# Kernel tuning notes

Hardware: AMD Instinct MI355X
Metric: run time of the kernel (lower is better)

The kernel has to match this reference:

```python
import jax, jax.numpy as jnp
import numpy as np

N = 50000      # nodes
E = 800000     # edges
IN = 64        # in_feats
HID = 4        # hidden_size
OUT = 64       # out_feats
COORS = 3
EPS = 1e-07
NEG_SLOPE = 0.01  # F.leaky_relu default


def setup_inputs() -> dict:
    key = jax.random.key(0)
    ks = jax.random.split(key, 10)
    feat = jax.random.normal(ks[0], (N, IN), dtype=jnp.float32)
    pos = jax.random.normal(ks[1], (N, COORS), dtype=jnp.float32)
    src = jax.random.randint(ks[2], (E,), 0, N, dtype=jnp.int32)
    dst = jax.random.randint(ks[3], (E,), 0, N, dtype=jnp.int32)
    W_self = jax.random.normal(ks[4], (OUT, IN), dtype=jnp.float32) * 0.1
    W_sp = jax.random.normal(ks[5], (HID * IN, COORS), dtype=jnp.float32) * 0.3
    b_sp = jax.random.normal(ks[6], (HID * IN,), dtype=jnp.float32) * 0.05
    W_neigh = jax.random.normal(ks[7], (OUT, HID * IN), dtype=jnp.float32) * 0.05
    b_neigh = jax.random.normal(ks[8], (OUT,), dtype=jnp.float32) * 0.05
    bias = jnp.zeros((OUT,), dtype=jnp.float32)
    return {"feat": feat, "pos": pos, "src": src, "dst": dst,
            "W_self": W_self, "W_sp": W_sp, "b_sp": b_sp,
            "W_neigh": W_neigh, "b_neigh": b_neigh, "bias": bias}


def reference(feat, pos, src, dst, W_self, W_sp, b_sp, W_neigh, b_neigh, bias):
    # per-edge spatial weighting
    rel = pos[dst] - pos[src]                                   # [E, 3]
    scal = jnp.linalg.norm(rel, axis=1, keepdims=True) + EPS    # [E, 1]
    ws = (rel + 1.0) / scal                                     # [E, 3]
    s = jax.nn.leaky_relu(ws @ W_sp.T + b_sp, NEG_SLOPE)        # [E, HID*IN]
    # modulate gathered src features: reshape(E, IN, HID) * h_src[:, :, None]
    msg = (s.reshape(E, IN, HID) * feat[src][:, :, None]).reshape(E, IN * HID)
    # mean aggregation per destination node (zero for isolated nodes)
    neigh_sum = jax.ops.segment_sum(msg, dst, num_segments=N)   # [N, IN*HID]
    cnt = jax.ops.segment_sum(jnp.ones((E,), feat.dtype), dst, num_segments=N)
    neigh_h = neigh_sum / jnp.maximum(cnt, 1.0)[:, None]
    # output projections
    h_neigh = neigh_h @ W_neigh.T + b_neigh                     # [N, OUT]
    rst = feat @ W_self.T + h_neigh + bias                      # [N, OUT]
    return rst
```

## Files before the change

kernel.cpp:

```cpp
#include <hip/hip_runtime.h>
#include <math.h>

#define N_NODES 50000
#define N_EDGES 800000
#define EPS 1e-7f
#define NEG_SLOPE 0.01f

#define BUCKET 64
#define GSTRIDE 72
#define EDGE_BLOCKS (N_EDGES / 256)
#define FEAT_BLOCKS (N_NODES * 64 / 4 / 256)

typedef __attribute__((ext_vector_type(8))) short short8;
typedef __attribute__((ext_vector_type(4))) float f32x4;

__device__ __forceinline__ unsigned bf16_rne(float x) {
    unsigned u = __float_as_uint(x);
    u += 0x7fffu + ((u >> 16) & 1u);
    return u >> 16;
}
__device__ __forceinline__ unsigned pack_bf16(float a, float b) {
    return bf16_rne(a) | (bf16_rne(b) << 16);
}


__global__ __launch_bounds__(256) void hist_geom_kernel(
    const int* __restrict__ src, const int* __restrict__ dst,
    const float* __restrict__ pos, int* __restrict__ cnt,
    uint2* __restrict__ gdata)
{
    const int i = blockIdx.x * 256 + threadIdx.x;
    const int s = src[i], d = dst[i];
    const float sx = pos[s * 3 + 0], sy = pos[s * 3 + 1], sz = pos[s * 3 + 2];
    const float dx = pos[d * 3 + 0], dy = pos[d * 3 + 1], dz = pos[d * 3 + 2];
    const float rx = dx - sx, ry = dy - sy, rz = dz - sz;
    const float inv =
        __builtin_amdgcn_rcpf(__builtin_amdgcn_sqrtf(rx * rx + ry * ry + rz * rz) + EPS);
    const uint2 rec = make_uint2(pack_bf16((rx + 1.f) * inv, (ry + 1.f) * inv),
                                 bf16_rne((rz + 1.f) * inv) | ((unsigned)s << 16));
    const int p = atomicAdd(&cnt[d], 1);
    if (p < BUCKET) gdata[(size_t)d * GSTRIDE + p] = rec;
}


__global__ __launch_bounds__(256) void featpack_kernel(
    const float* __restrict__ feat, uint2* __restrict__ featb2,
    const float* __restrict__ W_neigh, const float* __restrict__ W_self,
    const float* __restrict__ b_neigh, const float* __restrict__ bias,
    unsigned* __restrict__ wnp, unsigned* __restrict__ wsp, float* __restrict__ bb)
{
    const int bid = blockIdx.x;
    if (bid == FEAT_BLOCKS) {
        const int t = threadIdx.x;
        const float2* Wn2 = (const float2*)W_neigh;
        const float2* Ws2 = (const float2*)W_self;
        for (int i = t; i < 64 * 128; i += 256) {
            float2 v = Wn2[i];
            wnp[i] = pack_bf16(v.x, v.y);
        }
        for (int i = t; i < 64 * 32; i += 256) {
            float2 v = Ws2[i];
            wsp[i] = pack_bf16(v.x, v.y);
        }
        if (t < 64) bb[t] = b_neigh[t] + bias[t];
        return;
    }
    const int idx = bid * 256 + threadIdx.x;
    float4 v = reinterpret_cast<const float4*>(feat)[idx];
    featb2[idx] = make_uint2(pack_bf16(v.x, v.y), pack_bf16(v.z, v.w));
}


#define ACC_STRIDE 264

__device__ __forceinline__ float featload(const unsigned short* featb, unsigned rec_y, int lane) {
    return __uint_as_float((unsigned)featb[(size_t)(rec_y >> 16) * 64 + lane] << 16);
}

__global__ __launch_bounds__(256) void aggregate_project_kernel(
    const unsigned short* __restrict__ featb, const float* __restrict__ W_sp,
    const float* __restrict__ b_sp, const int* __restrict__ cnt,
    const uint2* __restrict__ gdata, const short* __restrict__ wnb,
    const short* __restrict__ wsb, const float* __restrict__ bb,
    float* __restrict__ out)
{
    __shared__ unsigned short accS[16 * ACC_STRIDE];
    __shared__ uint2 recS[16 * GSTRIDE];

    const int lane = threadIdx.x & 63;
    const int w = threadIdx.x >> 6;
    const int nb = blockIdx.x << 4;

    {
        const uint2* gsrc = gdata + (size_t)nb * GSTRIDE;
        for (int i = threadIdx.x; i < 16 * GSTRIDE; i += 256) recS[i] = gsrc[i];
    }

    float wsp0[4], wsp1[4], wsp2[4], bsp[4];
#pragma unroll
    for (int h = 0; h < 4; ++h) {
        int j = lane * 4 + h;
        wsp0[h] = W_sp[j * 3 + 0];
        wsp1[h] = W_sp[j * 3 + 1];
        wsp2[h] = W_sp[j * 3 + 2];
        bsp[h]  = b_sp[j];
    }
    __syncthreads();

#define MLP_ACC(U, F)                                                              \
    {                                                                              \
        const float wx = __uint_as_float((U).x << 16);                             \
        const float wy = __uint_as_float((U).x & 0xffff0000u);                     \
        const float wz = __uint_as_float((U).y << 16);                             \
        float t0 = fmaf(wx, wsp0[0], fmaf(wy, wsp1[0], fmaf(wz, wsp2[0], bsp[0])));\
        float t1 = fmaf(wx, wsp0[1], fmaf(wy, wsp1[1], fmaf(wz, wsp2[1], bsp[1])));\
        float t2 = fmaf(wx, wsp0[2], fmaf(wy, wsp1[2], fmaf(wz, wsp2[2], bsp[2])));\
        float t3 = fmaf(wx, wsp0[3], fmaf(wy, wsp1[3], fmaf(wz, wsp2[3], bsp[3])));\
        a0 = fmaf(fmaxf(t0, t0 * NEG_SLOPE), (F), a0);                             \
        a1 = fmaf(fmaxf(t1, t1 * NEG_SLOPE), (F), a1);                             \
        a2 = fmaf(fmaxf(t2, t2 * NEG_SLOPE), (F), a2);                             \
        a3 = fmaf(fmaxf(t3, t3 * NEG_SLOPE), (F), a3);                             \
    }

    for (int q = 0; q < 4; ++q) {
        const int r = (w << 2) + q;
        const int n = nb + r;
        const int degt = __builtin_amdgcn_readfirstlane(cnt[n]);
        const int deg = min(degt, BUCKET);
        const uint2* gp = &recS[r * GSTRIDE];

        float a0 = 0.f, a1 = 0.f, a2 = 0.f, a3 = 0.f;

        if (deg > 0) {
            const int dm = deg - 1;
            uint2 u0 = gp[0];
            uint2 u1 = gp[1];
            float f0 = featload(featb, u0.y, lane);
            float f1 = featload(featb, u1.y, lane);

            for (int e = 0; e < deg; e += 2) {
                uint2 u2 = gp[e + 2];
                uint2 u3 = gp[e + 3];
                float f2 = featload(featb, u2.y, lane);
                float f3 = featload(featb, u3.y, lane);

                MLP_ACC(u0, f0)
                {
                    const float fm = (e + 1 <= dm) ? f1 : 0.f;
                    MLP_ACC(u1, fm)
                }

                u0 = u2; u1 = u3;
                f0 = f2; f1 = f3;
            }
        }

        const float mscale = 1.f / fmaxf((float)degt, 1.f);
        uint2 pv = make_uint2(pack_bf16(a0 * mscale, a1 * mscale),
                              pack_bf16(a2 * mscale, a3 * mscale));
        *reinterpret_cast<uint2*>(&accS[r * ACC_STRIDE + lane * 4]) = pv;
    }
#undef MLP_ACC
    __syncthreads();

    const int mrow = lane & 15;
    const int quad = lane >> 4;
    const int o = (w << 4) + mrow;

    f32x4 acc = {0.f, 0.f, 0.f, 0.f};

    const unsigned short* Ar = &accS[mrow * ACC_STRIDE + quad * 8];
    const short* Br = wnb + o * 256 + quad * 8;
#pragma unroll
    for (int ks = 0; ks < 8; ++ks) {
        short8 a = *reinterpret_cast<const short8*>(Ar + ks * 32);
        short8 b = *reinterpret_cast<const short8*>(Br + ks * 32);
        acc = __builtin_amdgcn_mfma_f32_16x16x32_bf16(a, b, acc, 0, 0, 0);
    }

    const short* Fr = (const short*)featb + (size_t)(nb + mrow) * 64 + quad * 8;
    const short* Sr = wsb + o * 64 + quad * 8;
#pragma unroll
    for (int ks = 0; ks < 2; ++ks) {
        short8 a = *reinterpret_cast<const short8*>(Fr + ks * 32);
        short8 b = *reinterpret_cast<const short8*>(Sr + ks * 32);
        acc = __builtin_amdgcn_mfma_f32_16x16x32_bf16(a, b, acc, 0, 0, 0);
    }

    const float badd = bb[o];
#pragma unroll
    for (int r = 0; r < 4; ++r) {
        out[(size_t)(nb + quad * 4 + r) * 64 + o] = acc[r] + badd;
    }
}


extern "C" void kernel_launch(void* const* d_in, const int* in_sizes, int n_in,
                              void* d_out, int out_size, void* d_ws, size_t ws_size,
                              hipStream_t stream) {
    (void)in_sizes; (void)n_in; (void)out_size; (void)ws_size;
    const float* feat    = (const float*)d_in[0];
    const float* pos     = (const float*)d_in[1];
    const int*   src     = (const int*)d_in[2];
    const int*   dst     = (const int*)d_in[3];
    const float* W_self  = (const float*)d_in[4];
    const float* W_sp    = (const float*)d_in[5];
    const float* b_sp    = (const float*)d_in[6];
    const float* W_neigh = (const float*)d_in[7];
    const float* b_neigh = (const float*)d_in[8];
    const float* bias    = (const float*)d_in[9];
    float* out = (float*)d_out;

    uint2*        gdata  = (uint2*)d_ws;
    uint2*        featb2 = gdata + (size_t)N_NODES * GSTRIDE;
    unsigned int* wnp    = (unsigned int*)(featb2 + 800000);
    unsigned int* wsp    = wnp + 8192;
    float*        bb     = (float*)(wsp + 2048);
    int*          cnt    = (int*)(bb + 64);

    hipMemsetAsync(cnt, 0, (size_t)N_NODES * sizeof(int), stream);
    featpack_kernel<<<FEAT_BLOCKS + 1, 256, 0, stream>>>(
        feat, featb2, W_neigh, W_self, b_neigh, bias, wnp, wsp, bb);
    hist_geom_kernel<<<EDGE_BLOCKS, 256, 0, stream>>>(src, dst, pos, cnt, gdata);
    aggregate_project_kernel<<<N_NODES / 16, 256, 0, stream>>>(
        (const unsigned short*)featb2, W_sp, b_sp, cnt, gdata,
        (const short*)wnp, (const short*)wsp, bb, out);
}
```

Baseline: 185.1 us.

## Store 16-bit source ids in buckets and compute edge geometry in aggregation

The histogram pass now scatters only a 16-bit source index per edge instead of an 8-byte record with precomputed geometry. The relative-position weighting is recomputed inside the aggregation kernel, one edge per lane, and staged in shared memory. The feature-pack and histogram kernels are also merged into a single launch. This shrinks the random scatter traffic and the bucket reads and drops one launch, at the cost of extra pos gathers and math in the aggregation kernel.

```diff
diff --git a/kernel.cpp b/kernel.cpp
--- a/kernel.cpp
+++ b/kernel.cpp
@@ -8,8 +8,9 @@
 
 #define BUCKET 64
 #define GSTRIDE 72
+#define FEAT_BLOCKS (N_NODES * 64 / 4 / 256)
 #define EDGE_BLOCKS (N_EDGES / 256)
-#define FEAT_BLOCKS (N_NODES * 64 / 4 / 256)
+#define ACC_STRIDE 264
 
 typedef __attribute__((ext_vector_type(8))) short short8;
 typedef __attribute__((ext_vector_type(4))) float f32x4;
@@ -24,32 +25,21 @@
 }
 
 
-__global__ __launch_bounds__(256) void hist_geom_kernel(
-    const int* __restrict__ src, const int* __restrict__ dst,
-    const float* __restrict__ pos, int* __restrict__ cnt,
-    uint2* __restrict__ gdata)
-{
-    const int i = blockIdx.x * 256 + threadIdx.x;
-    const int s = src[i], d = dst[i];
-    const float sx = pos[s * 3 + 0], sy = pos[s * 3 + 1], sz = pos[s * 3 + 2];
-    const float dx = pos[d * 3 + 0], dy = pos[d * 3 + 1], dz = pos[d * 3 + 2];
-    const float rx = dx - sx, ry = dy - sy, rz = dz - sz;
-    const float inv =
-        __builtin_amdgcn_rcpf(__builtin_amdgcn_sqrtf(rx * rx + ry * ry + rz * rz) + EPS);
-    const uint2 rec = make_uint2(pack_bf16((rx + 1.f) * inv, (ry + 1.f) * inv),
-                                 bf16_rne((rz + 1.f) * inv) | ((unsigned)s << 16));
-    const int p = atomicAdd(&cnt[d], 1);
-    if (p < BUCKET) gdata[(size_t)d * GSTRIDE + p] = rec;
-}
-
-
-__global__ __launch_bounds__(256) void featpack_kernel(
+__global__ __launch_bounds__(256) void pack_hist_kernel(
     const float* __restrict__ feat, uint2* __restrict__ featb2,
     const float* __restrict__ W_neigh, const float* __restrict__ W_self,
     const float* __restrict__ b_neigh, const float* __restrict__ bias,
-    unsigned* __restrict__ wnp, unsigned* __restrict__ wsp, float* __restrict__ bb)
+    unsigned* __restrict__ wnp, unsigned* __restrict__ wsp, float* __restrict__ bb,
+    const int* __restrict__ src, const int* __restrict__ dst,
+    int* __restrict__ cnt, unsigned short* __restrict__ gsrcs)
 {
     const int bid = blockIdx.x;
+    if (bid < FEAT_BLOCKS) {
+        const int idx = bid * 256 + threadIdx.x;
+        float4 v = reinterpret_cast<const float4*>(feat)[idx];
+        featb2[idx] = make_uint2(pack_bf16(v.x, v.y), pack_bf16(v.z, v.w));
+        return;
+    }
     if (bid == FEAT_BLOCKS) {
         const int t = threadIdx.x;
         const float2* Wn2 = (const float2*)W_neigh;
@@ -65,36 +55,32 @@
         if (t < 64) bb[t] = b_neigh[t] + bias[t];
         return;
     }
-    const int idx = bid * 256 + threadIdx.x;
-    float4 v = reinterpret_cast<const float4*>(feat)[idx];
-    featb2[idx] = make_uint2(pack_bf16(v.x, v.y), pack_bf16(v.z, v.w));
-}
-
-
-#define ACC_STRIDE 264
-
-__device__ __forceinline__ float featload(const unsigned short* featb, unsigned rec_y, int lane) {
-    return __uint_as_float((unsigned)featb[(size_t)(rec_y >> 16) * 64 + lane] << 16);
+    const int i = (bid - FEAT_BLOCKS - 1) * 256 + threadIdx.x;
+    const int s = src[i], d = dst[i];
+    const int p = atomicAdd(&cnt[d], 1);
+    if (p < BUCKET) gsrcs[(size_t)d * GSTRIDE + p] = (unsigned short)s;
+}
+
+
+__device__ __forceinline__ float featload(const unsigned short* featb, unsigned rec_y,
+                                          int lane) {
+    const unsigned idx = ((rec_y >> 10) & 0x3FFFC0u) + (unsigned)lane;
+    return __uint_as_float((unsigned)featb[idx] << 16);
 }
 
 __global__ __launch_bounds__(256) void aggregate_project_kernel(
     const unsigned short* __restrict__ featb, const float* __restrict__ W_sp,
     const float* __restrict__ b_sp, const int* __restrict__ cnt,
-    const uint2* __restrict__ gdata, const short* __restrict__ wnb,
-    const short* __restrict__ wsb, const float* __restrict__ bb,
-    float* __restrict__ out)
+    const unsigned short* __restrict__ gsrcs, const float* __restrict__ pos,
+    const short* __restrict__ wnb, const short* __restrict__ wsb,
+    const float* __restrict__ bb, float* __restrict__ out)
 {
     __shared__ unsigned short accS[16 * ACC_STRIDE];
-    __shared__ uint2 recS[16 * GSTRIDE];
+    __shared__ uint2 recG[16 * GSTRIDE];
 
     const int lane = threadIdx.x & 63;
     const int w = threadIdx.x >> 6;
     const int nb = blockIdx.x << 4;
-
-    {
-        const uint2* gsrc = gdata + (size_t)nb * GSTRIDE;
-        for (int i = threadIdx.x; i < 16 * GSTRIDE; i += 256) recS[i] = gsrc[i];
-    }
 
     float wsp0[4], wsp1[4], wsp2[4], bsp[4];
 #pragma unroll
@@ -105,7 +91,28 @@
         wsp2[h] = W_sp[j * 3 + 2];
         bsp[h]  = b_sp[j];
     }
-    __syncthreads();
+
+    int degt[4];
+#pragma unroll
+    for (int q = 0; q < 4; ++q) {
+        const int r = (w << 2) + q;
+        const int n = nb + r;
+        degt[q] = cnt[n];
+        const int deg = min(degt[q], BUCKET);
+        uint2 rec = make_uint2(0u, 0u);
+        if (lane < deg) {
+            const int s = (int)gsrcs[(size_t)n * GSTRIDE + lane];
+            const float rx = pos[n * 3 + 0] - pos[s * 3 + 0];
+            const float ry = pos[n * 3 + 1] - pos[s * 3 + 1];
+            const float rz = pos[n * 3 + 2] - pos[s * 3 + 2];
+            const float inv = __builtin_amdgcn_rcpf(
+                __builtin_amdgcn_sqrtf(rx * rx + ry * ry + rz * rz) + EPS);
+            rec = make_uint2(pack_bf16((rx + 1.f) * inv, (ry + 1.f) * inv),
+                             bf16_rne((rz + 1.f) * inv) | ((unsigned)s << 16));
+        }
+        recG[r * GSTRIDE + lane] = rec;
+        if (lane < 8) recG[r * GSTRIDE + 64 + lane] = make_uint2(0u, 0u);
+    }
 
 #define MLP_ACC(U, F)                                                              \
     {                                                                              \
@@ -122,12 +129,12 @@
         a3 = fmaf(fmaxf(t3, t3 * NEG_SLOPE), (F), a3);                             \
     }
 
+#pragma unroll
     for (int q = 0; q < 4; ++q) {
         const int r = (w << 2) + q;
-        const int n = nb + r;
-        const int degt = __builtin_amdgcn_readfirstlane(cnt[n]);
-        const int deg = min(degt, BUCKET);
-        const uint2* gp = &recS[r * GSTRIDE];
+        const int dt = __builtin_amdgcn_readfirstlane(degt[q]);
+        const int deg = min(dt, BUCKET);
+        const uint2* gp = &recG[r * GSTRIDE];
 
         float a0 = 0.f, a1 = 0.f, a2 = 0.f, a3 = 0.f;
 
@@ -155,7 +162,7 @@
             }
         }
 
-        const float mscale = 1.f / fmaxf((float)degt, 1.f);
+        const float mscale = 1.f / fmaxf((float)dt, 1.f);
         uint2 pv = make_uint2(pack_bf16(a0 * mscale, a1 * mscale),
                               pack_bf16(a2 * mscale, a3 * mscale));
         *reinterpret_cast<uint2*>(&accS[r * ACC_STRIDE + lane * 4]) = pv;
@@ -211,18 +218,18 @@
     const float* bias    = (const float*)d_in[9];
     float* out = (float*)d_out;
 
-    uint2*        gdata  = (uint2*)d_ws;
-    uint2*        featb2 = gdata + (size_t)N_NODES * GSTRIDE;
-    unsigned int* wnp    = (unsigned int*)(featb2 + 800000);
-    unsigned int* wsp    = wnp + 8192;
-    float*        bb     = (float*)(wsp + 2048);
-    int*          cnt    = (int*)(bb + 64);
+    unsigned short* gsrcs  = (unsigned short*)d_ws;
+    uint2*          featb2 = (uint2*)(gsrcs + (size_t)N_NODES * GSTRIDE);
+    unsigned int*   wnp    = (unsigned int*)(featb2 + 800000);
+    unsigned int*   wsp    = wnp + 8192;
+    float*          bb     = (float*)(wsp + 2048);
+    int*            cnt    = (int*)(bb + 64);
 
     hipMemsetAsync(cnt, 0, (size_t)N_NODES * sizeof(int), stream);
-    featpack_kernel<<<FEAT_BLOCKS + 1, 256, 0, stream>>>(
-        feat, featb2, W_neigh, W_self, b_neigh, bias, wnp, wsp, bb);
-    hist_geom_kernel<<<EDGE_BLOCKS, 256, 0, stream>>>(src, dst, pos, cnt, gdata);
+    pack_hist_kernel<<<FEAT_BLOCKS + 1 + EDGE_BLOCKS, 256, 0, stream>>>(
+        feat, featb2, W_neigh, W_self, b_neigh, bias, wnp, wsp, bb,
+        src, dst, cnt, gsrcs);
     aggregate_project_kernel<<<N_NODES / 16, 256, 0, stream>>>(
-        (const unsigned short*)featb2, W_sp, b_sp, cnt, gdata,
+        (const unsigned short*)featb2, W_sp, b_sp, cnt, gsrcs, pos,
         (const short*)wnp, (const short*)wsp, bb, out);
 }
```

Measured after the change: 197.5 us. +6.7%, slower.
